# Kernel tuning notes

Hardware: AMD Instinct MI355X
Metric: run time of the kernel (lower is better)

Reference implementation:

```python
import jax, jax.numpy as jnp
import numpy as np

RHO = 0.1

def setup_inputs() -> dict:
    key = jax.random.key(0)
    k1, k2 = jax.random.split(key)
    B, C, H, W = 64, 256, 56, 56
    features = jax.random.normal(k1, (B, C, H, W), dtype=jnp.float32)
    grad = jax.random.normal(k2, (B, C, H, W), dtype=jnp.float32)
    return {"features": features, "grad": grad}


def reference(features, grad):
    # attribution = relu(grad * features), elementwise
    attribution = jax.nn.relu(grad * features)
    B = attribution.shape[0]
    flat_attr = attribution.reshape(B, -1)          # [B, C*H*W]
    k = int(RHO * flat_attr.shape[1])               # static: 80281
    topk_val, _ = jax.lax.top_k(flat_attr, k)       # [B, k], descending
    threshold = topk_val[:, -1].reshape(-1, 1, 1, 1)  # k-th largest per sample
    mask = (attribution <= threshold).astype(features.dtype)
    return features * mask
```

## Files before the change

kernel.cpp:

```cpp
#include <hip/hip_runtime.h>

namespace {
constexpr int NS   = 64;
constexpr int NPS  = 802816;
constexpr int NPSV = NPS / 4;
constexpr unsigned KSEL = 80281u;
constexpr unsigned SENT = 0xFFFFFFFFu;
constexpr int NB   = 8192;
constexpr int GX   = 16;
constexpr int TPB  = 49;
constexpr int PAIRCAP = 2048;
constexpr int CAP_LDS = 20480;
constexpr int BRB  = 8;
constexpr int CHUNKS = 128;
constexpr int CH_STRIDE = NPSV / CHUNKS;
constexpr unsigned RU_RANK = 12129u;
constexpr unsigned RL_RANK = 14086u;
constexpr int GXF  = 32;
constexpr int SEGVF = NPSV / GXF;
constexpr int SEGF  = NPS / GXF;
constexpr int GXA  = 64;
constexpr int SEGCAP2 = 20736;
constexpr int TAILF4  = 1056;
typedef float f32x4 __attribute__((ext_vector_type(4)));
}

__device__ __forceinline__ void nt_store4(float4* dst, const float4& v) {
    f32x4 w; w.x = v.x; w.y = v.y; w.z = v.z; w.w = v.w;
    __builtin_nontemporal_store(w, reinterpret_cast<f32x4*>(dst));
}

template <int NBINS>
__device__ void select_in_lds(const unsigned* __restrict__ h, unsigned K,
                              unsigned* bin, unsigned* rem) {
    constexpr int BPT = NBINS / 256;
    __shared__ unsigned cs[256];
    __shared__ unsigned fB, fR;
    const int t = threadIdx.x;
    unsigned s = 0;
    for (int j = 0; j < BPT; ++j) s += h[t * BPT + j];
    cs[t] = s;
    if (t == 0) { fB = SENT; fR = 0u; }
    __syncthreads();
    unsigned suf = 0;
    for (int j = t + 1; j < 256; ++j) suf += cs[j];
    if (suf < K && suf + s >= K) {
        unsigned cur = suf;
        for (int j = BPT - 1; j >= 0; --j) {
            const unsigned c = h[t * BPT + j];
            if (cur < K && cur + c >= K) { fB = (unsigned)(t * BPT + j); fR = K - cur; break; }
            cur += c;
        }
    }
    __syncthreads();
    const unsigned rb = fB, rr = fR;
    __syncthreads();
    *bin = rb; *rem = rr;
}

__global__ __launch_bounds__(256) void bracket_kernel(const float4* __restrict__ f,
                                                      const float4* __restrict__ g,
                                                      unsigned short* __restrict__ bh,
                                                      unsigned* __restrict__ fail) {
    __shared__ unsigned h[NB];
    const int jb = blockIdx.x, b = blockIdx.y, t = threadIdx.x;
    if (jb == 0 && b == 0 && t == 0) fail[0] = 0u;
    for (int k = t; k < NB; k += 256) h[k] = 0u;
    __syncthreads();
    const size_t base = (size_t)b * NPSV;
#define HBIN(p) { if ((p) > 0.0f) atomicAdd(&h[__float_as_uint(p) >> 18], 1u); }
    for (int c = 0; c < CHUNKS / BRB; c += 2) {
        const int ch = jb * (CHUNKS / BRB) + c;
        const size_t i0 = base + (size_t)ch * CH_STRIDE + t;
        const size_t i1 = base + (size_t)(ch + 1) * CH_STRIDE + t;
        const float4 fa = f[i0], fb = f[i1];
        const float4 ga = g[i0], gb = g[i1];
        HBIN(fa.x * ga.x) HBIN(fa.y * ga.y) HBIN(fa.z * ga.z) HBIN(fa.w * ga.w)
        HBIN(fb.x * gb.x) HBIN(fb.y * gb.y) HBIN(fb.z * gb.z) HBIN(fb.w * gb.w)
    }
#undef HBIN
    __syncthreads();
    unsigned short* o = bh + (size_t)(b * BRB + jb) * NB;
    for (int k = t; k < NB; k += 256) o[k] = (unsigned short)h[k];
}

__global__ __launch_bounds__(256) void bracket_scan_kernel(const unsigned short* __restrict__ bh,
                                                           unsigned* __restrict__ binLU) {
    __shared__ unsigned h[NB];
    const int b = blockIdx.x, t = threadIdx.x;
    for (int k = t; k < NB; k += 256) {
        unsigned s = 0;
        const unsigned short* p = bh + (size_t)b * BRB * NB + k;
        for (int j = 0; j < BRB; ++j) s += p[(size_t)j * NB];
        h[k] = s;
    }
    __syncthreads();
    unsigned bU, rU, bL, rL;
    select_in_lds<NB>(h, RU_RANK, &bU, &rU);
    select_in_lds<NB>(h, RL_RANK, &bL, &rL);
    if (t == 0) {
        binLU[2 * b]     = (bL == SENT) ? 0u : bL;
        binLU[2 * b + 1] = (bU == SENT) ? (unsigned)(NB - 1) : bU;
    }
}

__global__ __launch_bounds__(256) void scatter0_kernel(const float4* __restrict__ f,
                                                       const float4* __restrict__ g,
                                                       float4* __restrict__ out,
                                                       unsigned* __restrict__ pv,
                                                       unsigned* __restrict__ ppos,
                                                       const unsigned* __restrict__ binLU,
                                                       unsigned* __restrict__ cnts,
                                                       unsigned* __restrict__ chis,
                                                       unsigned* __restrict__ fail) {
    const int j = blockIdx.x, b = blockIdx.y, t = threadIdx.x;
    const unsigned binL = binLU[2 * b], binU = binLU[2 * b + 1];
    __shared__ unsigned cnt;
    __shared__ unsigned wsum[4];
    __shared__ unsigned lv[PAIRCAP];
    __shared__ unsigned lp[PAIRCAP];
    if (t == 0) cnt = 0u;
    __syncthreads();
    const size_t sbase = (size_t)b * NPSV;
    unsigned chi = 0;
#define PROC(FC, GC, IDX, CIDX, OC) { \
        const float p_ = (FC) * (GC); \
        const unsigned u_ = __float_as_uint(p_); \
        const unsigned pre_ = u_ >> 18; \
        const bool pos_ = p_ > 0.0f; \
        const bool drop_ = pos_ && (pre_ > binU); \
        OC = drop_ ? 0.0f : (FC); \
        chi += drop_; \
        if (pos_ && pre_ >= binL && pre_ <= binU) { \
            const unsigned x_ = atomicAdd(&cnt, 1u); \
            if (x_ < PAIRCAP) { lv[x_] = u_; lp[x_] = (unsigned)((IDX) * 4) + CIDX; } \
        } }
#define PROC4(FV, GV, IDX, OV) \
        PROC(FV.x, GV.x, IDX, 0u, OV.x) PROC(FV.y, GV.y, IDX, 1u, OV.y) \
        PROC(FV.z, GV.z, IDX, 2u, OV.z) PROC(FV.w, GV.w, IDX, 3u, OV.w)

    for (int k = 0; k < TPB; ++k) {
        const int i = (k * GX + j) * 256 + t;
        const float4 fv = f[sbase + i];
        const float4 gv = g[sbase + i];
        float4 o;
        PROC4(fv, gv, i, o)
        nt_store4(&out[sbase + i], o);
    }
#undef PROC4
#undef PROC
    for (int off = 32; off; off >>= 1) chi += __shfl_down(chi, off);
    if ((t & 63) == 0) wsum[t >> 6] = chi;
    __syncthreads();
    const unsigned ctot = cnt;
    const unsigned c = (ctot > PAIRCAP) ? PAIRCAP : ctot;
    const size_t segp = (size_t)(b * GX + j) * PAIRCAP;
    for (unsigned k = t; k < c; k += 256) { pv[segp + k] = lv[k]; ppos[segp + k] = lp[k]; }
    if (t == 0) {
        chis[b * GX + j] = wsum[0] + wsum[1] + wsum[2] + wsum[3];
        cnts[b * GX + j] = c;
        if (ctot > PAIRCAP) fail[0] = 1u;
    }
}

__global__ __launch_bounds__(256) void select0_kernel(const unsigned* __restrict__ pv,
                                                      const unsigned* __restrict__ ppos,
                                                      const unsigned* __restrict__ binLU,
                                                      const unsigned* __restrict__ cnts,
                                                      const unsigned* __restrict__ chis,
                                                      unsigned* __restrict__ fail,
                                                      float* __restrict__ thrF,
                                                      float* __restrict__ out) {
    if (fail[0]) return;
    const int b = blockIdx.x, t = threadIdx.x;
    __shared__ unsigned vals[CAP_LDS];
    __shared__ unsigned hist[NB];
    __shared__ unsigned soff[GX + 1];
    __shared__ unsigned sh_chi;
    __shared__ float sh_thr;
    if (t == 0) {
        unsigned o = 0;
        for (int j = 0; j < GX; ++j) { soff[j] = o; o += cnts[b * GX + j]; }
        soff[GX] = o;
        unsigned c = 0;
        for (int j = 0; j < GX; ++j) c += chis[b * GX + j];
        sh_chi = c;
    }
    __syncthreads();
    const unsigned ncand = soff[GX];
    const unsigned chi = sh_chi;
    if (chi >= KSEL) { if (t == 0) fail[0] = 1u; return; }
    if (ncand > CAP_LDS) { if (t == 0) fail[0] = 1u; return; }
    const unsigned Krem = KSEL - chi;
    bool zeroThr = false;
    if (Krem > ncand) {
        if (binLU[2 * b] == 0u) zeroThr = true;
        else { if (t == 0) fail[0] = 1u; return; }
    }
    for (int j = 0; j < GX; ++j) {
        const unsigned c = soff[j + 1] - soff[j];
        const unsigned* s = pv + (size_t)(b * GX + j) * PAIRCAP;
        for (unsigned i = t; i < c; i += 256) vals[soff[j] + i] = s[i];
    }
    if (zeroThr) {
        if (t == 0) { sh_thr = 0.0f; thrF[b] = 0.0f; }
        __syncthreads();
    } else {
        for (int k = t; k < NB; k += 256) hist[k] = 0u;
        __syncthreads();
        for (unsigned i = t; i < ncand; i += 256) atomicAdd(&hist[vals[i] >> 18], 1u);
        __syncthreads();
        unsigned P1, r1; select_in_lds<NB>(hist, Krem, &P1, &r1);
        __syncthreads();
        for (int k = t; k < NB; k += 256) hist[k] = 0u;
        __syncthreads();
        for (unsigned i = t; i < ncand; i += 256) {
            const unsigned u = vals[i];
            if ((u >> 18) == P1) atomicAdd(&hist[(u >> 5) & (NB - 1u)], 1u);
        }
        __syncthreads();
        unsigned P2, r2; select_in_lds<NB>(hist, r1, &P2, &r2);
        __syncthreads();
        if (t < 32) hist[t] = 0u;
        __syncthreads();
        const unsigned pref = (P1 << 13) | P2;
        for (unsigned i = t; i < ncand; i += 256) {
            const unsigned u = vals[i];
            if ((u >> 5) == pref) atomicAdd(&hist[u & 31u], 1u);
        }
        __syncthreads();
        if (t == 0) {
            unsigned cur = 0, b3 = 0;
            for (int q = 31; q >= 0; --q) {
                const unsigned c = hist[q];
                if (cur < r2 && cur + c >= r2) { b3 = (unsigned)q; break; }
                cur += c;
            }
            const float thr = __uint_as_float((P1 << 18) | (P2 << 5) | b3);
            sh_thr = thr; thrF[b] = thr;
        }
        __syncthreads();
    }
    const float thr = sh_thr;
    float* ob = out + (size_t)b * NPS;
    for (int j = 0; j < GX; ++j) {
        const unsigned c = soff[j + 1] - soff[j];
        const unsigned* qp = ppos + (size_t)(b * GX + j) * PAIRCAP;
        const unsigned so = soff[j];
        for (unsigned i = t; i < c; i += 256) {
            if (__uint_as_float(vals[so + i]) > thr) ob[qp[i]] = 0.0f;
        }
    }
}

__global__ __launch_bounds__(256) void scatter_fb_kernel(const float4* __restrict__ f,
                                                         const float4* __restrict__ g,
                                                         unsigned* __restrict__ list,
                                                         unsigned* __restrict__ cnts,
                                                         unsigned* __restrict__ chis,
                                                         const unsigned* __restrict__ fail,
                                                         int mode, int segCap) {
    if (mode == 1 && fail[0] == 0u) return;
    const int j = blockIdx.x, b = blockIdx.y, t = threadIdx.x;
    __shared__ unsigned cnt;
    if (t == 0) cnt = 0u;
    __syncthreads();
    unsigned* __restrict__ seg = list + (size_t)b * NPS + (size_t)j * SEGF;
    const size_t base = (size_t)b * NPSV + (size_t)j * SEGVF;
    for (int i = t; i < SEGVF; i += 256) {
        const float4 fv = f[base + i];
        const float4 gv = g[base + i];
        const float p0 = fv.x * gv.x, p1 = fv.y * gv.y, p2 = fv.z * gv.z, p3 = fv.w * gv.w;
#define PROCF(p) { if ((p) > 0.0f) { const unsigned x = atomicAdd(&cnt, 1u); \
                   if ((int)x < segCap) seg[x] = __float_as_uint(p); } }
        PROCF(p0) PROCF(p1) PROCF(p2) PROCF(p3)
#undef PROCF
    }
    __syncthreads();
    if (t == 0) {
        cnts[b * GXF + j] = (cnt > (unsigned)segCap) ? (unsigned)segCap : cnt;
        chis[b * GXF + j] = 0u;
    }
}

__global__ __launch_bounds__(256) void select_fb_kernel(const unsigned* __restrict__ list,
                                                        const unsigned* __restrict__ cnts,
                                                        unsigned* __restrict__ fail,
                                                        float* __restrict__ thrF,
                                                        int mode) {
    if (mode == 1 && fail[0] == 0u) return;
    const int b = blockIdx.x, t = threadIdx.x;
    __shared__ unsigned h[NB];
    __shared__ unsigned segc[GXF];
    if (t < GXF) segc[t] = cnts[b * GXF + t];
    __syncthreads();
    unsigned ncand = 0;
    for (int j = 0; j < GXF; ++j) ncand += segc[j];
    if (KSEL > ncand) {
        if (t == 0) thrF[b] = 0.0f;
        return;
    }
    const unsigned* __restrict__ seg0 = list + (size_t)b * NPS;
    for (int k = t; k < NB; k += 256) h[k] = 0u;
    __syncthreads();
    for (int j = 0; j < GXF; ++j) {
        const unsigned c = segc[j];
        const unsigned* s = seg0 + (size_t)j * SEGF;
        for (unsigned i = t; i < c; i += 256) atomicAdd(&h[s[i] >> 18], 1u);
    }
    __syncthreads();
    unsigned P1, r1; select_in_lds<NB>(h, KSEL, &P1, &r1);
    __syncthreads();
    for (int k = t; k < NB; k += 256) h[k] = 0u;
    __syncthreads();
    for (int j = 0; j < GXF; ++j) {
        const unsigned c = segc[j];
        const unsigned* s = seg0 + (size_t)j * SEGF;
        for (unsigned i = t; i < c; i += 256) {
            const unsigned u = s[i];
            if ((u >> 18) == P1) atomicAdd(&h[(u >> 5) & (NB - 1u)], 1u);
        }
    }
    __syncthreads();
    unsigned P2, r2; select_in_lds<NB>(h, r1, &P2, &r2);
    __syncthreads();
    if (t < 32) h[t] = 0u;
    __syncthreads();
    const unsigned pref = (P1 << 13) | P2;
    for (int j = 0; j < GXF; ++j) {
        const unsigned c = segc[j];
        const unsigned* s = seg0 + (size_t)j * SEGF;
        for (unsigned i = t; i < c; i += 256) {
            const unsigned u = s[i];
            if ((u >> 5) == pref) atomicAdd(&h[u & 31u], 1u);
        }
    }
    __syncthreads();
    if (t == 0) {
        unsigned cur = 0, b3 = 0;
        for (int q = 31; q >= 0; --q) {
            const unsigned c = h[q];
            if (cur < r2 && cur + c >= r2) { b3 = (unsigned)q; break; }
            cur += c;
        }
        thrF[b] = __uint_as_float((P1 << 18) | (P2 << 5) | b3);
    }
}

__global__ __launch_bounds__(256) void apply_fb_kernel(const float4* __restrict__ f,
                                                       const float4* __restrict__ g,
                                                       const float* __restrict__ thrF,
                                                       float4* __restrict__ out,
                                                       const unsigned* __restrict__ fail,
                                                       int mode, int tailCut) {
    if (mode == 1 && fail[0] == 0u) return;
    const int b = blockIdx.y;
    const float thr = thrF[b];
    const size_t base = (size_t)b * NPSV;
    const int limit = NPSV - ((b == NS - 1) ? tailCut : 0);
    const int stride = gridDim.x * blockDim.x;
    for (int i = blockIdx.x * 256 + threadIdx.x; i < limit; i += stride) {
        const float4 fv = f[base + i];
        const float4 gv = g[base + i];
        float4 o;
        o.x = (fv.x * gv.x > thr) ? 0.0f : fv.x;
        o.y = (fv.y * gv.y > thr) ? 0.0f : fv.y;
        o.z = (fv.z * gv.z > thr) ? 0.0f : fv.z;
        o.w = (fv.w * gv.w > thr) ? 0.0f : fv.w;
        out[base + i] = o;
    }
}

__global__ void apply_tail_kernel(const float4* __restrict__ f, const float4* __restrict__ g,
                                  const float* __restrict__ thrF,
                                  float4* __restrict__ out, int tailCut) {
    const float thr = thrF[NS - 1];
    asm volatile("" :: "v"(thr));
    __syncthreads();
    const size_t base = (size_t)NS * NPSV - tailCut;
    for (int i = threadIdx.x; i < tailCut; i += 256) {
        const float4 fv = f[base + i];
        const float4 gv = g[base + i];
        float4 o;
        o.x = (fv.x * gv.x > thr) ? 0.0f : fv.x;
        o.y = (fv.y * gv.y > thr) ? 0.0f : fv.y;
        o.z = (fv.z * gv.z > thr) ? 0.0f : fv.z;
        o.w = (fv.w * gv.w > thr) ? 0.0f : fv.w;
        out[base + i] = o;
    }
}

extern "C" void kernel_launch(void* const* d_in, const int* in_sizes, int n_in,
                              void* d_out, int out_size, void* d_ws, size_t ws_size,
                              hipStream_t stream) {
    const float* f = (const float*)d_in[0];
    const float* g = (const float*)d_in[1];
    float* out = (float*)d_out;

    const size_t pairU32  = (size_t)NS * GX * PAIRCAP;
    const size_t brBytes  = (size_t)NS * BRB * NB * sizeof(unsigned short);
    const size_t bigBytes = (pairU32 * 8 > brBytes) ? pairU32 * 8 : brBytes;
    const size_t smallU32 = 2 * NS + NS * GXF + NS * GXF + 1 + NS;
    const size_t need     = bigBytes + smallU32 * 4;

    if (ws_size >= need) {
        char* w = (char*)d_ws;
        unsigned short* bh = (unsigned short*)w;
        unsigned* pv   = (unsigned*)w;
        unsigned* ppos = pv + pairU32;
        unsigned* sm   = (unsigned*)(w + bigBytes);
        unsigned* binLU = sm;
        unsigned* cnts  = binLU + 2 * NS;
        unsigned* chis  = cnts + NS * GXF;
        unsigned* fail  = chis + NS * GXF;
        float*    thrF  = (float*)(fail + 1);

        bracket_kernel<<<dim3(BRB, NS), 256, 0, stream>>>((const float4*)f, (const float4*)g,
                                                          bh, fail);
        bracket_scan_kernel<<<NS, 256, 0, stream>>>(bh, binLU);
        scatter0_kernel<<<dim3(GX, NS), 256, 0, stream>>>((const float4*)f, (const float4*)g,
                                                          (float4*)out, pv, ppos, binLU,
                                                          cnts, chis, fail);
        select0_kernel<<<NS, 256, 0, stream>>>(pv, ppos, binLU, cnts, chis, fail, thrF, out);
        scatter_fb_kernel<<<dim3(GXF, NS), 256, 0, stream>>>((const float4*)f, (const float4*)g,
                                                             (unsigned*)out, cnts, chis, fail,
                                                             1, SEGF);
        select_fb_kernel<<<NS, 256, 0, stream>>>((const unsigned*)out, cnts, fail, thrF, 1);
        apply_fb_kernel<<<dim3(GXA, NS), 256, 0, stream>>>((const float4*)f, (const float4*)g,
                                                           thrF, (float4*)out, fail, 1, 0);
    } else {
        unsigned* list = (unsigned*)out;
        unsigned* sm   = (unsigned*)out + ((size_t)NS * NPS - 4 * TAILF4);
        unsigned* cnts = sm;
        unsigned* chis = cnts + NS * GXF;
        unsigned* fail = chis + NS * GXF;
        float*    thrF = (float*)(fail + 1);

        scatter_fb_kernel<<<dim3(GXF, NS), 256, 0, stream>>>((const float4*)f, (const float4*)g,
                                                             list, cnts, chis, fail, 2, SEGCAP2);
        select_fb_kernel<<<NS, 256, 0, stream>>>(list, cnts, fail, thrF, 2);
        apply_fb_kernel<<<dim3(GXA, NS), 256, 0, stream>>>((const float4*)f, (const float4*)g,
                                                           thrF, (float4*)out, fail, 2, TAILF4);
        apply_tail_kernel<<<1, 256, 0, stream>>>((const float4*)f, (const float4*)g,
                                                 thrF, (float4*)out, TAILF4);
    }
}
```

Measured before the change: 219.8 us.

## Collapse fallback path into one exact per-sample kernel, vectorize bracket histogram merge

Replaces the three fallback kernels (scatter, select, apply) and the tail kernel with a single per-sample fb_exact_kernel that recomputes the radix histograms directly from features and gradients, with no intermediate candidate list. On the main path this removes two no-op launches that only checked the fail flag. It also vectorizes the merge of the 16-bit bracket histograms in bracket_scan_kernel and switches the scatter0 output from nontemporal to normal stores. The fallback becomes slower when it does trigger: it uses one block per sample and makes up to four full passes over the inputs.

```diff
diff --git a/kernel.cpp b/kernel.cpp
--- a/kernel.cpp
+++ b/kernel.cpp
@@ -16,18 +16,6 @@
 constexpr int CH_STRIDE = NPSV / CHUNKS;
 constexpr unsigned RU_RANK = 12129u;
 constexpr unsigned RL_RANK = 14086u;
-constexpr int GXF  = 32;
-constexpr int SEGVF = NPSV / GXF;
-constexpr int SEGF  = NPS / GXF;
-constexpr int GXA  = 64;
-constexpr int SEGCAP2 = 20736;
-constexpr int TAILF4  = 1056;
-typedef float f32x4 __attribute__((ext_vector_type(4)));
-}
-
-__device__ __forceinline__ void nt_store4(float4* dst, const float4& v) {
-    f32x4 w; w.x = v.x; w.y = v.y; w.z = v.z; w.w = v.w;
-    __builtin_nontemporal_store(w, reinterpret_cast<f32x4*>(dst));
 }
 
 template <int NBINS>
@@ -88,11 +76,17 @@
                                                            unsigned* __restrict__ binLU) {
     __shared__ unsigned h[NB];
     const int b = blockIdx.x, t = threadIdx.x;
-    for (int k = t; k < NB; k += 256) {
-        unsigned s = 0;
-        const unsigned short* p = bh + (size_t)b * BRB * NB + k;
-        for (int j = 0; j < BRB; ++j) s += p[(size_t)j * NB];
-        h[k] = s;
+    for (int grp = t; grp < NB / 8; grp += 256) {
+        unsigned acc[8] = {0, 0, 0, 0, 0, 0, 0, 0};
+        for (int j = 0; j < BRB; ++j) {
+            const uint4 v = *reinterpret_cast<const uint4*>(
+                bh + (size_t)(b * BRB + j) * NB + grp * 8);
+            acc[0] += v.x & 0xFFFFu; acc[1] += v.x >> 16;
+            acc[2] += v.y & 0xFFFFu; acc[3] += v.y >> 16;
+            acc[4] += v.z & 0xFFFFu; acc[5] += v.z >> 16;
+            acc[6] += v.w & 0xFFFFu; acc[7] += v.w >> 16;
+        }
+        for (int e = 0; e < 8; ++e) h[grp * 8 + e] = acc[e];
     }
     __syncthreads();
     unsigned bU, rU, bL, rL;
@@ -145,7 +139,7 @@
         const float4 gv = g[sbase + i];
         float4 o;
         PROC4(fv, gv, i, o)
-        nt_store4(&out[sbase + i], o);
+        out[sbase + i] = o;
     }
 #undef PROC4
 #undef PROC
@@ -253,113 +247,70 @@
     }
 }
 
-__global__ __launch_bounds__(256) void scatter_fb_kernel(const float4* __restrict__ f,
-                                                         const float4* __restrict__ g,
-                                                         unsigned* __restrict__ list,
-                                                         unsigned* __restrict__ cnts,
-                                                         unsigned* __restrict__ chis,
-                                                         const unsigned* __restrict__ fail,
-                                                         int mode, int segCap) {
-    if (mode == 1 && fail[0] == 0u) return;
-    const int j = blockIdx.x, b = blockIdx.y, t = threadIdx.x;
-    __shared__ unsigned cnt;
-    if (t == 0) cnt = 0u;
-    __syncthreads();
-    unsigned* __restrict__ seg = list + (size_t)b * NPS + (size_t)j * SEGF;
-    const size_t base = (size_t)b * NPSV + (size_t)j * SEGVF;
-    for (int i = t; i < SEGVF; i += 256) {
-        const float4 fv = f[base + i];
-        const float4 gv = g[base + i];
-        const float p0 = fv.x * gv.x, p1 = fv.y * gv.y, p2 = fv.z * gv.z, p3 = fv.w * gv.w;
-#define PROCF(p) { if ((p) > 0.0f) { const unsigned x = atomicAdd(&cnt, 1u); \
-                   if ((int)x < segCap) seg[x] = __float_as_uint(p); } }
-        PROCF(p0) PROCF(p1) PROCF(p2) PROCF(p3)
-#undef PROCF
-    }
-    __syncthreads();
-    if (t == 0) {
-        cnts[b * GXF + j] = (cnt > (unsigned)segCap) ? (unsigned)segCap : cnt;
-        chis[b * GXF + j] = 0u;
-    }
-}
-
-__global__ __launch_bounds__(256) void select_fb_kernel(const unsigned* __restrict__ list,
-                                                        const unsigned* __restrict__ cnts,
-                                                        unsigned* __restrict__ fail,
-                                                        float* __restrict__ thrF,
-                                                        int mode) {
+__global__ __launch_bounds__(256) void fb_exact_kernel(const float4* __restrict__ f,
+                                                       const float4* __restrict__ g,
+                                                       float4* __restrict__ out,
+                                                       const unsigned* __restrict__ fail,
+                                                       int mode) {
     if (mode == 1 && fail[0] == 0u) return;
     const int b = blockIdx.x, t = threadIdx.x;
     __shared__ unsigned h[NB];
-    __shared__ unsigned segc[GXF];
-    if (t < GXF) segc[t] = cnts[b * GXF + t];
-    __syncthreads();
-    unsigned ncand = 0;
-    for (int j = 0; j < GXF; ++j) ncand += segc[j];
-    if (KSEL > ncand) {
-        if (t == 0) thrF[b] = 0.0f;
-        return;
-    }
-    const unsigned* __restrict__ seg0 = list + (size_t)b * NPS;
+    __shared__ float sthr;
+    const size_t base = (size_t)b * NPSV;
     for (int k = t; k < NB; k += 256) h[k] = 0u;
     __syncthreads();
-    for (int j = 0; j < GXF; ++j) {
-        const unsigned c = segc[j];
-        const unsigned* s = seg0 + (size_t)j * SEGF;
-        for (unsigned i = t; i < c; i += 256) atomicAdd(&h[s[i] >> 18], 1u);
+    for (int i = t; i < NPSV; i += 256) {
+        const float4 fv = f[base + i];
+        const float4 gv = g[base + i];
+#define H1(p) { if ((p) > 0.0f) atomicAdd(&h[__float_as_uint(p) >> 18], 1u); }
+        H1(fv.x * gv.x) H1(fv.y * gv.y) H1(fv.z * gv.z) H1(fv.w * gv.w)
+#undef H1
     }
     __syncthreads();
     unsigned P1, r1; select_in_lds<NB>(h, KSEL, &P1, &r1);
     __syncthreads();
-    for (int k = t; k < NB; k += 256) h[k] = 0u;
-    __syncthreads();
-    for (int j = 0; j < GXF; ++j) {
-        const unsigned c = segc[j];
-        const unsigned* s = seg0 + (size_t)j * SEGF;
-        for (unsigned i = t; i < c; i += 256) {
-            const unsigned u = s[i];
-            if ((u >> 18) == P1) atomicAdd(&h[(u >> 5) & (NB - 1u)], 1u);
-        }
-    }
-    __syncthreads();
-    unsigned P2, r2; select_in_lds<NB>(h, r1, &P2, &r2);
-    __syncthreads();
-    if (t < 32) h[t] = 0u;
-    __syncthreads();
-    const unsigned pref = (P1 << 13) | P2;
-    for (int j = 0; j < GXF; ++j) {
-        const unsigned c = segc[j];
-        const unsigned* s = seg0 + (size_t)j * SEGF;
-        for (unsigned i = t; i < c; i += 256) {
-            const unsigned u = s[i];
-            if ((u >> 5) == pref) atomicAdd(&h[u & 31u], 1u);
-        }
-    }
-    __syncthreads();
-    if (t == 0) {
-        unsigned cur = 0, b3 = 0;
-        for (int q = 31; q >= 0; --q) {
-            const unsigned c = h[q];
-            if (cur < r2 && cur + c >= r2) { b3 = (unsigned)q; break; }
-            cur += c;
-        }
-        thrF[b] = __uint_as_float((P1 << 18) | (P2 << 5) | b3);
-    }
-}
-
-__global__ __launch_bounds__(256) void apply_fb_kernel(const float4* __restrict__ f,
-                                                       const float4* __restrict__ g,
-                                                       const float* __restrict__ thrF,
-                                                       float4* __restrict__ out,
-                                                       const unsigned* __restrict__ fail,
-                                                       int mode, int tailCut) {
-    if (mode == 1 && fail[0] == 0u) return;
-    const int b = blockIdx.y;
-    const float thr = thrF[b];
-    const size_t base = (size_t)b * NPSV;
-    const int limit = NPSV - ((b == NS - 1) ? tailCut : 0);
-    const int stride = gridDim.x * blockDim.x;
-    for (int i = blockIdx.x * 256 + threadIdx.x; i < limit; i += stride) {
+    if (P1 == SENT) {
+        if (t == 0) sthr = 0.0f;
+        __syncthreads();
+    } else {
+        for (int k = t; k < NB; k += 256) h[k] = 0u;
+        __syncthreads();
+        for (int i = t; i < NPSV; i += 256) {
+            const float4 fv = f[base + i];
+            const float4 gv = g[base + i];
+#define H2(p) { if ((p) > 0.0f) { const unsigned u = __float_as_uint(p); \
+                if ((u >> 18) == P1) atomicAdd(&h[(u >> 5) & (NB - 1u)], 1u); } }
+            H2(fv.x * gv.x) H2(fv.y * gv.y) H2(fv.z * gv.z) H2(fv.w * gv.w)
+#undef H2
+        }
+        __syncthreads();
+        unsigned P2, r2; select_in_lds<NB>(h, r1, &P2, &r2);
+        __syncthreads();
+        if (t < 32) h[t] = 0u;
+        __syncthreads();
+        const unsigned pref = (P1 << 13) | P2;
+        for (int i = t; i < NPSV; i += 256) {
+            const float4 fv = f[base + i];
+            const float4 gv = g[base + i];
+#define H3(p) { if ((p) > 0.0f) { const unsigned u = __float_as_uint(p); \
+                if ((u >> 5) == pref) atomicAdd(&h[u & 31u], 1u); } }
+            H3(fv.x * gv.x) H3(fv.y * gv.y) H3(fv.z * gv.z) H3(fv.w * gv.w)
+#undef H3
+        }
+        __syncthreads();
+        if (t == 0) {
+            unsigned cur = 0, b3 = 0;
+            for (int q = 31; q >= 0; --q) {
+                const unsigned c = h[q];
+                if (cur < r2 && cur + c >= r2) { b3 = (unsigned)q; break; }
+                cur += c;
+            }
+            sthr = __uint_as_float((P1 << 18) | (P2 << 5) | b3);
+        }
+        __syncthreads();
+    }
+    const float thr = sthr;
+    for (int i = t; i < NPSV; i += 256) {
         const float4 fv = f[base + i];
         const float4 gv = g[base + i];
         float4 o;
@@ -371,25 +322,6 @@
     }
 }
 
-__global__ void apply_tail_kernel(const float4* __restrict__ f, const float4* __restrict__ g,
-                                  const float* __restrict__ thrF,
-                                  float4* __restrict__ out, int tailCut) {
-    const float thr = thrF[NS - 1];
-    asm volatile("" :: "v"(thr));
-    __syncthreads();
-    const size_t base = (size_t)NS * NPSV - tailCut;
-    for (int i = threadIdx.x; i < tailCut; i += 256) {
-        const float4 fv = f[base + i];
-        const float4 gv = g[base + i];
-        float4 o;
-        o.x = (fv.x * gv.x > thr) ? 0.0f : fv.x;
-        o.y = (fv.y * gv.y > thr) ? 0.0f : fv.y;
-        o.z = (fv.z * gv.z > thr) ? 0.0f : fv.z;
-        o.w = (fv.w * gv.w > thr) ? 0.0f : fv.w;
-        out[base + i] = o;
-    }
-}
-
 extern "C" void kernel_launch(void* const* d_in, const int* in_sizes, int n_in,
                               void* d_out, int out_size, void* d_ws, size_t ws_size,
                               hipStream_t stream) {
@@ -400,7 +332,7 @@
     const size_t pairU32  = (size_t)NS * GX * PAIRCAP;
     const size_t brBytes  = (size_t)NS * BRB * NB * sizeof(unsigned short);
     const size_t bigBytes = (pairU32 * 8 > brBytes) ? pairU32 * 8 : brBytes;
-    const size_t smallU32 = 2 * NS + NS * GXF + NS * GXF + 1 + NS;
+    const size_t smallU32 = 2 * NS + NS * GX + NS * GX + 1 + NS;
     const size_t need     = bigBytes + smallU32 * 4;
 
     if (ws_size >= need) {
@@ -411,8 +343,8 @@
         unsigned* sm   = (unsigned*)(w + bigBytes);
         unsigned* binLU = sm;
         unsigned* cnts  = binLU + 2 * NS;
-        unsigned* chis  = cnts + NS * GXF;
-        unsigned* fail  = chis + NS * GXF;
+        unsigned* chis  = cnts + NS * GX;
+        unsigned* fail  = chis + NS * GX;
         float*    thrF  = (float*)(fail + 1);
 
         bracket_kernel<<<dim3(BRB, NS), 256, 0, stream>>>((const float4*)f, (const float4*)g,
@@ -422,26 +354,10 @@
                                                           (float4*)out, pv, ppos, binLU,
                                                           cnts, chis, fail);
         select0_kernel<<<NS, 256, 0, stream>>>(pv, ppos, binLU, cnts, chis, fail, thrF, out);
-        scatter_fb_kernel<<<dim3(GXF, NS), 256, 0, stream>>>((const float4*)f, (const float4*)g,
-                                                             (unsigned*)out, cnts, chis, fail,
-                                                             1, SEGF);
-        select_fb_kernel<<<NS, 256, 0, stream>>>((const unsigned*)out, cnts, fail, thrF, 1);
-        apply_fb_kernel<<<dim3(GXA, NS), 256, 0, stream>>>((const float4*)f, (const float4*)g,
-                                                           thrF, (float4*)out, fail, 1, 0);
+        fb_exact_kernel<<<NS, 256, 0, stream>>>((const float4*)f, (const float4*)g,
+                                                (float4*)out, fail, 1);
     } else {
-        unsigned* list = (unsigned*)out;
-        unsigned* sm   = (unsigned*)out + ((size_t)NS * NPS - 4 * TAILF4);
-        unsigned* cnts = sm;
-        unsigned* chis = cnts + NS * GXF;
-        unsigned* fail = chis + NS * GXF;
-        float*    thrF = (float*)(fail + 1);
-
-        scatter_fb_kernel<<<dim3(GXF, NS), 256, 0, stream>>>((const float4*)f, (const float4*)g,
-                                                             list, cnts, chis, fail, 2, SEGCAP2);
-        select_fb_kernel<<<NS, 256, 0, stream>>>(list, cnts, fail, thrF, 2);
-        apply_fb_kernel<<<dim3(GXA, NS), 256, 0, stream>>>((const float4*)f, (const float4*)g,
-                                                           thrF, (float4*)out, fail, 2, TAILF4);
-        apply_tail_kernel<<<1, 256, 0, stream>>>((const float4*)f, (const float4*)g,
-                                                 thrF, (float4*)out, TAILF4);
-    }
-}
+        fb_exact_kernel<<<NS, 256, 0, stream>>>((const float4*)f, (const float4*)g,
+                                                (float4*)out, (const unsigned*)d_out, 2);
+    }
+}
```

New measurement: 236.7 us. 1.08x slower.
